# Performance work log

Measured on AMD Instinct MI355X. Metric: run time of the kernel, lower is better.

The kernel has to match this reference:

```python
import jax, jax.numpy as jnp
import numpy as np

B, L, H = 2, 2048, 1024
N_HEADS = 16
HEAD = H // N_HEADS
LN_EPS = 1e-12


def setup_inputs() -> dict:
    key = jax.random.key(0)
    ks = jax.random.split(key, 8)
    s = 1.0 / np.sqrt(H)
    return {
        "embeddings": jax.random.normal(ks[0], (B, L, H), dtype=jnp.float32),
        "mask": jnp.zeros((B, 1, 1, L), dtype=jnp.float32),
        "Wq": jax.random.normal(ks[1], (H, H), dtype=jnp.float32) * s,
        "bq": jnp.zeros((H,), dtype=jnp.float32),
        "Wk": jax.random.normal(ks[2], (H, H), dtype=jnp.float32) * s,
        "bk": jnp.zeros((H,), dtype=jnp.float32),
        "Wv": jax.random.normal(ks[3], (H, H), dtype=jnp.float32) * s,
        "bv": jnp.zeros((H,), dtype=jnp.float32),
        "Wo": jax.random.normal(ks[4], (H, H), dtype=jnp.float32) * s,
        "bo": jnp.zeros((H,), dtype=jnp.float32),
        "ln_gamma": jnp.ones((H,), dtype=jnp.float32),
        "ln_beta": jnp.zeros((H,), dtype=jnp.float32),
    }


def _layer_norm(x, gamma, beta):
    mu = jnp.mean(x, axis=-1, keepdims=True)
    var = jnp.mean(jnp.square(x - mu), axis=-1, keepdims=True)
    return (x - mu) * jax.lax.rsqrt(var + LN_EPS) * gamma + beta


def reference(embeddings, mask, Wq, bq, Wk, bk, Wv, bv, Wo, bo, ln_gamma, ln_beta):
    b, l, h = embeddings.shape
    # QKV projections, split heads -> [b, n_heads, l, head]
    def split_heads(x):
        return x.reshape(b, l, N_HEADS, HEAD).transpose(0, 2, 1, 3)
    q = split_heads(embeddings @ Wq + bq)
    k = split_heads(embeddings @ Wk + bk)
    v = split_heads(embeddings @ Wv + bv)
    # Faithful to source: energies use Q @ V^T, scaled by sqrt(n_heads)
    energies = jnp.einsum("bhqd,bhkd->bhqk", q, v) / np.sqrt(N_HEADS) + mask
    weights = jax.nn.softmax(energies, axis=3)
    # Faithful to source: attended = weights @ K
    attended = jnp.einsum("bhqk,bhkd->bhqd", weights, k)
    attended = attended.transpose(0, 2, 1, 3).reshape(b, l, h)
    # Residual feed-forward (BertSelfOutput style): dense + residual + LN
    out = attended @ Wo + bo
    return _layer_norm(out + embeddings, ln_gamma, ln_beta)
```

## Files before the change

kernel.cpp:

```cpp
#include <hip/hip_runtime.h>

#define LOG2E 1.44269504f
#define C_QSCALE 0.360673760f
#define C_SHIFT  34.6246810f
typedef unsigned short u16;
typedef short bf16x8 __attribute__((ext_vector_type(8)));
typedef float f32x4 __attribute__((ext_vector_type(4)));
typedef unsigned short u16x4 __attribute__((ext_vector_type(4)));

#define BB 2
#define LL 2048
#define HH 1024
#define NH 16
#define HD 64
#define ML (BB*LL)

__device__ __forceinline__ u16 f2bf(float f) {
  union { float f; unsigned u; } v; v.f = f;
  unsigned r = v.u + 0x7FFFu + ((v.u >> 16) & 1u);
  return (u16)(r >> 16);
}
__device__ __forceinline__ u16 f2bf_trunc(float f) {
  union { float f; unsigned u; } v; v.f = f;
  return (u16)(v.u >> 16);
}
__device__ __forceinline__ void gload_lds16(const u16* g, u16* l) {
  __builtin_amdgcn_global_load_lds((const __attribute__((address_space(1))) void*)g,
                                   (__attribute__((address_space(3))) void*)l, 16, 0, 0);
}

__global__ __launch_bounds__(256) void k_convert(const float* __restrict__ E, u16* __restrict__ X) {
  int idx = (blockIdx.x * 256 + threadIdx.x) * 8;
  float4 a = *(const float4*)(E + idx);
  float4 b = *(const float4*)(E + idx + 4);
  bf16x8 o;
  o[0]=f2bf(a.x); o[1]=f2bf(a.y); o[2]=f2bf(a.z); o[3]=f2bf(a.w);
  o[4]=f2bf(b.x); o[5]=f2bf(b.y); o[6]=f2bf(b.z); o[7]=f2bf(b.w);
  *(bf16x8*)(X + idx) = o;
}

__global__ __launch_bounds__(256) void k_transpose(const float* W0, const float* W1,
                                                   const float* W2, const float* W3,
                                                   u16* __restrict__ WT) {
  const float* W = (blockIdx.z==0)?W0:(blockIdx.z==1)?W1:(blockIdx.z==2)?W2:W3;
  u16* dst = WT + (size_t)blockIdx.z * HH * HH;
  __shared__ __align__(16) u16 T[64*72];
  int t = threadIdx.x;
  int n0 = blockIdx.x * 64, k0 = blockIdx.y * 64;
  int kl = t >> 2, nc = t & 3;
  #pragma unroll
  for (int u = 0; u < 4; ++u) {
    float4 v = *(const float4*)(W + (size_t)(k0 + kl) * HH + n0 + nc*16 + u*4);
    int nb = nc*16 + u*4;
    T[(nb+0)*72 + kl] = f2bf(v.x);
    T[(nb+1)*72 + kl] = f2bf(v.y);
    T[(nb+2)*72 + kl] = f2bf(v.z);
    T[(nb+3)*72 + kl] = f2bf(v.w);
  }
  __syncthreads();
  int nl = t >> 2, kc = (t & 3) * 16;
  #pragma unroll
  for (int e = 0; e < 2; ++e) {
    bf16x8 v = *(const bf16x8*)(T + nl*72 + kc + e*8);
    *(bf16x8*)(dst + (size_t)(n0+nl)*HH + k0 + kc + e*8) = v;
  }
}

__global__ __launch_bounds__(256) void k_gemm(const u16* __restrict__ A, const u16* __restrict__ Bt,
                                              const float* __restrict__ b0, const float* __restrict__ b1,
                                              const float* __restrict__ b2,
                                              u16* __restrict__ QH, u16* __restrict__ KV,
                                              float* __restrict__ outf, int mode) {
  __shared__ __align__(16) u16 As[128*32];
  __shared__ __align__(16) u16 Bs[128*32];
  int tid = threadIdx.x;
  int lane = tid & 63, w = tid >> 6;
  int c = lane & 15, g = lane >> 4;
  int bn0 = blockIdx.x * 128, bm0 = blockIdx.y * 128;
  int wm0 = (w >> 1) * 64, wn0 = (w & 1) * 64;
  f32x4 acc[4][4];
  #pragma unroll
  for (int mt = 0; mt < 4; ++mt)
    #pragma unroll
    for (int nt = 0; nt < 4; ++nt)
      acc[mt][nt] = (f32x4){0.f,0.f,0.f,0.f};

  for (int kt = 0; kt < 32; ++kt) {
    int k0 = kt * 32;
    __syncthreads();
    #pragma unroll
    for (int it = 0; it < 2; ++it) {
      int ch = tid + it*256;
      int row = ch >> 2, col = (ch & 3) * 8;
      gload_lds16(A  + (size_t)(bm0 + row) * HH + k0 + col, As + ch*8);
      gload_lds16(Bt + (size_t)(bn0 + row) * HH + k0 + col, Bs + ch*8);
    }
    __syncthreads();
    bf16x8 af[4], bfr[4];
    #pragma unroll
    for (int i = 0; i < 4; ++i) {
      af[i]  = *(const bf16x8*)(As + (wm0 + i*16 + c)*32 + g*8);
      bfr[i] = *(const bf16x8*)(Bs + (wn0 + i*16 + c)*32 + g*8);
    }
    #pragma unroll
    for (int mt = 0; mt < 4; ++mt)
      #pragma unroll
      for (int nt = 0; nt < 4; ++nt)
        acc[mt][nt] = __builtin_amdgcn_mfma_f32_16x16x32_bf16(af[mt], bfr[nt], acc[mt][nt], 0, 0, 0);
  }
  #pragma unroll
  for (int nt = 0; nt < 4; ++nt) {
    int n = bn0 + wn0 + nt*16 + c;
    if (mode == 1) {
      float bv = b0[n];
      #pragma unroll
      for (int mt = 0; mt < 4; ++mt) {
        int m0 = bm0 + wm0 + mt*16 + 4*g;
        #pragma unroll
        for (int r = 0; r < 4; ++r)
          outf[(size_t)(m0 + r) * HH + n] = acc[mt][nt][r] + bv;
      }
    } else {
      int z = n >> 10;
      int nn = n & 1023, h = nn >> 6, d = nn & 63;
      const float* bp = (z == 0) ? b0 : (z == 1) ? b1 : b2;
      float bv = bp[nn];
      #pragma unroll
      for (int mt = 0; mt < 4; ++mt) {
        int m0 = bm0 + wm0 + mt*16 + 4*g;
        int b = m0 >> 11;
        if (z == 0) {
          #pragma unroll
          for (int r = 0; r < 4; ++r) {
            int l = (m0 + r) & 2047;
            QH[(((size_t)(b*NH + h)) * LL + l) * HD + d] = f2bf(acc[mt][nt][r] + bv);
          }
        } else if (z == 1) {
          int keyl = m0 & 2047;
          int t = keyl >> 6, chunk = (keyl >> 3) & 7, s = keyl & 7;
          u16x4 pk;
          #pragma unroll
          for (int r = 0; r < 4; ++r) pk[r] = f2bf(acc[mt][nt][r] + bv);
          size_t addr = ((size_t)((b*NH + h)*32 + t))*8192 + d*64 + ((chunk ^ (d & 7))*8) + s;
          *(u16x4*)(KV + addr) = pk;
        } else {
          #pragma unroll
          for (int r = 0; r < 4; ++r) {
            int vl = (m0 + r) & 2047;
            int t = vl >> 6;
            size_t addr = ((size_t)((b*NH + h)*32 + t))*8192 + 4096
                        + (vl & 63)*64 + (((d >> 3) ^ (vl & 7))*8) + (d & 7);
            KV[addr] = f2bf(acc[mt][nt][r] + bv);
          }
        }
      }
    }
  }
}

__global__ __launch_bounds__(256) void k_attn(const u16* __restrict__ QH, const u16* __restrict__ KV,
                                              const float* __restrict__ mask, u16* __restrict__ ATT) {
  __shared__ __align__(16) u16 sKV[8192];
  __shared__ __align__(16) u16 sP[4][32*72];
  int tid = threadIdx.x;
  int lane = tid & 63, w = tid >> 6;
  int c = lane & 15, g = lane >> 4;
  int bh = blockIdx.y, b = bh >> 4, h = bh & 15;
  int q0 = blockIdx.x * 128 + w * 32;
  size_t qbase = (size_t)bh * LL * HD;
  const u16* kvg = KV + (size_t)bh * 32 * 8192;
  const float* mptr = mask + b * LL;

  bf16x8 aq[2][2];
  #pragma unroll
  for (int qi = 0; qi < 2; ++qi)
    #pragma unroll
    for (int ks = 0; ks < 2; ++ks)
      aq[qi][ks] = *(const bf16x8*)(QH + qbase + (size_t)(q0 + qi*16 + c) * HD + ks*32 + g*8);

  bf16x8 ones;
  #pragma unroll
  for (int i = 0; i < 8; ++i) ones[i] = (short)0x3F80;

  f32x4 O[2][4], lac[2];
  #pragma unroll
  for (int qi = 0; qi < 2; ++qi) {
    lac[qi] = (f32x4){0.f,0.f,0.f,0.f};
    #pragma unroll
    for (int dt = 0; dt < 4; ++dt) O[qi][dt] = (f32x4){0.f,0.f,0.f,0.f};
  }
  u16* pw = &sP[w][0];

  for (int t = 0; t < 32; ++t) {
    int kv0 = t * 64;
    __syncthreads();
    #pragma unroll
    for (int it = 0; it < 4; ++it) {
      int i = tid + it*256;
      gload_lds16(kvg + (size_t)t*8192 + i*8, sKV + i*8);
    }
    __syncthreads();

    #pragma unroll
    for (int nt = 0; nt < 4; ++nt) {
      int vrow = nt*16 + c;
      bf16x8 vb0 = *(const bf16x8*)(sKV + 4096 + vrow*64 + ((g ^ (c & 7))*8));
      bf16x8 vb1 = *(const bf16x8*)(sKV + 4096 + vrow*64 + (((4 + g) ^ (c & 7))*8));
      float mterm = fmaf(mptr[kv0 + nt*16 + c], LOG2E, -C_SHIFT);
      #pragma unroll
      for (int qi = 0; qi < 2; ++qi) {
        f32x4 sa = (f32x4){0.f,0.f,0.f,0.f};
        sa = __builtin_amdgcn_mfma_f32_16x16x32_bf16(aq[qi][0], vb0, sa, 0,0,0);
        sa = __builtin_amdgcn_mfma_f32_16x16x32_bf16(aq[qi][1], vb1, sa, 0,0,0);
        #pragma unroll
        for (int r = 0; r < 4; ++r) {
          float p = exp2f(fmaf(sa[r], C_QSCALE, mterm));
          pw[(qi*16 + 4*g + r)*72 + nt*16 + c] = f2bf_trunc(p);
        }
      }
    }
    bf16x8 ap[2][2];
    #pragma unroll
    for (int qi = 0; qi < 2; ++qi) {
      #pragma unroll
      for (int ks = 0; ks < 2; ++ks)
        ap[qi][ks] = *(const bf16x8*)(pw + (qi*16 + c)*72 + ks*32 + g*8);
      lac[qi] = __builtin_amdgcn_mfma_f32_16x16x32_bf16(ap[qi][0], ones, lac[qi], 0,0,0);
      lac[qi] = __builtin_amdgcn_mfma_f32_16x16x32_bf16(ap[qi][1], ones, lac[qi], 0,0,0);
    }
    #pragma unroll
    for (int dt = 0; dt < 4; ++dt) {
      int d = dt*16 + c;
      bf16x8 bk0 = *(const bf16x8*)(sKV + d*64 + ((g ^ (c & 7))*8));
      bf16x8 bk1 = *(const bf16x8*)(sKV + d*64 + (((4 + g) ^ (c & 7))*8));
      #pragma unroll
      for (int qi = 0; qi < 2; ++qi) {
        O[qi][dt] = __builtin_amdgcn_mfma_f32_16x16x32_bf16(ap[qi][0], bk0, O[qi][dt], 0,0,0);
        O[qi][dt] = __builtin_amdgcn_mfma_f32_16x16x32_bf16(ap[qi][1], bk1, O[qi][dt], 0,0,0);
      }
    }
  }
  #pragma unroll
  for (int qi = 0; qi < 2; ++qi)
    #pragma unroll
    for (int r = 0; r < 4; ++r) {
      float inv = 1.0f / lac[qi][r];
      int q = q0 + qi*16 + 4*g + r;
      #pragma unroll
      for (int dt = 0; dt < 4; ++dt)
        ATT[((size_t)(b*LL + q)) * HH + h*HD + dt*16 + c] = f2bf(O[qi][dt][r] * inv);
    }
}

__global__ __launch_bounds__(256) void k_ln(const float* __restrict__ OF, const float* __restrict__ E,
                                            const float* __restrict__ gamma, const float* __restrict__ beta,
                                            float* __restrict__ out) {
  int row = blockIdx.x;
  int tid = threadIdx.x, lane = tid & 63, w = tid >> 6;
  size_t basei = (size_t)row * HH + tid*4;
  float4 a = *(const float4*)(OF + basei);
  float4 e = *(const float4*)(E + basei);
  float x0 = a.x + e.x, x1 = a.y + e.y, x2 = a.z + e.z, x3 = a.w + e.w;
  float s1 = x0+x1+x2+x3;
  float s2 = x0*x0+x1*x1+x2*x2+x3*x3;
  #pragma unroll
  for (int off = 32; off; off >>= 1) { s1 += __shfl_xor(s1, off); s2 += __shfl_xor(s2, off); }
  __shared__ float r1[4], r2[4];
  if (lane == 0) { r1[w] = s1; r2[w] = s2; }
  __syncthreads();
  s1 = r1[0]+r1[1]+r1[2]+r1[3];
  s2 = r2[0]+r2[1]+r2[2]+r2[3];
  float mu = s1 * (1.0f/HH);
  float var = s2 * (1.0f/HH) - mu*mu;
  float rs = rsqrtf(fmaxf(var, 0.f) + 1e-12f);
  int colb = tid*4;
  float4 gm = *(const float4*)(gamma + colb);
  float4 bt = *(const float4*)(beta + colb);
  float4 o;
  o.x = (x0-mu)*rs*gm.x + bt.x;
  o.y = (x1-mu)*rs*gm.y + bt.y;
  o.z = (x2-mu)*rs*gm.z + bt.z;
  o.w = (x3-mu)*rs*gm.w + bt.w;
  *(float4*)(out + basei) = o;
}

extern "C" void kernel_launch(void* const* d_in, const int* in_sizes, int n_in,
                              void* d_out, int out_size, void* d_ws, size_t ws_size,
                              hipStream_t stream) {
  const float* E    = (const float*)d_in[0];
  const float* mask = (const float*)d_in[1];
  const float* Wq   = (const float*)d_in[2];
  const float* bq   = (const float*)d_in[3];
  const float* Wk   = (const float*)d_in[4];
  const float* bk   = (const float*)d_in[5];
  const float* Wv   = (const float*)d_in[6];
  const float* bv   = (const float*)d_in[7];
  const float* Wo   = (const float*)d_in[8];
  const float* bo   = (const float*)d_in[9];
  const float* gam  = (const float*)d_in[10];
  const float* bet  = (const float*)d_in[11];

  const size_t MH = (size_t)ML * HH;
  u16* XBF = (u16*)d_ws;
  u16* WT  = XBF + MH;
  u16* QH  = WT + 4*(size_t)HH*HH;
  u16* KV  = QH + MH;
  u16* ATT = KV + 2*MH;
  float* OF = (float*)QH;
  float* out = (float*)d_out;

  k_convert<<<dim3(ML*HH/(256*8)), 256, 0, stream>>>(E, XBF);
  k_transpose<<<dim3(16,16,4), 256, 0, stream>>>(Wq, Wk, Wv, Wo, WT);
  k_gemm<<<dim3(24,32), 256, 0, stream>>>(XBF, WT, bq, bk, bv, QH, KV, nullptr, 0);
  k_attn<<<dim3(16,32), 256, 0, stream>>>(QH, KV, mask, ATT);
  k_gemm<<<dim3(8,32), 256, 0, stream>>>(ATT, WT + 3*(size_t)HH*HH, bo, nullptr, nullptr,
                                         nullptr, nullptr, OF, 1);
  k_ln<<<dim3(ML), 256, 0, stream>>>(OF, E, gam, bet, out);
}
```

Measured before the change: 273.1 us.

## Double-buffer GEMM and attention loads, merge prep kernels, vectorize epilogue stores

Merges the bf16 conversion and weight transpose into one prep launch. Double-buffers the LDS tiles in the GEMM and the KV tiles in attention, so the next tile's global-to-LDS load overlaps the current tile's MFMA work and one barrier per iteration goes away. The GEMM swaps operands for the Q/V/output projections so the epilogue can write packed 4-wide stores. Attention is reworked to 16 queries per wave with twice the blocks, using transposed MFMA operands so outputs are stored as packed vectors. The costs are double the LDS footprint per block, and the prefetch is issued after only a single barrier, which may rely on implicit waits for the async loads to be safe.

```diff
diff --git a/kernel.cpp b/kernel.cpp
--- a/kernel.cpp
+++ b/kernel.cpp
@@ -29,24 +29,27 @@
                                    (__attribute__((address_space(3))) void*)l, 16, 0, 0);
 }
 
-__global__ __launch_bounds__(256) void k_convert(const float* __restrict__ E, u16* __restrict__ X) {
-  int idx = (blockIdx.x * 256 + threadIdx.x) * 8;
-  float4 a = *(const float4*)(E + idx);
-  float4 b = *(const float4*)(E + idx + 4);
-  bf16x8 o;
-  o[0]=f2bf(a.x); o[1]=f2bf(a.y); o[2]=f2bf(a.z); o[3]=f2bf(a.w);
-  o[4]=f2bf(b.x); o[5]=f2bf(b.y); o[6]=f2bf(b.z); o[7]=f2bf(b.w);
-  *(bf16x8*)(X + idx) = o;
-}
-
-__global__ __launch_bounds__(256) void k_transpose(const float* W0, const float* W1,
-                                                   const float* W2, const float* W3,
-                                                   u16* __restrict__ WT) {
-  const float* W = (blockIdx.z==0)?W0:(blockIdx.z==1)?W1:(blockIdx.z==2)?W2:W3;
-  u16* dst = WT + (size_t)blockIdx.z * HH * HH;
+__global__ __launch_bounds__(256) void k_prep(const float* __restrict__ E, u16* __restrict__ X,
+                                              const float* W0, const float* W1,
+                                              const float* W2, const float* W3,
+                                              u16* __restrict__ WT) {
   __shared__ __align__(16) u16 T[64*72];
+  if (blockIdx.x < 2048) {
+    int idx = (blockIdx.x * 256 + threadIdx.x) * 8;
+    float4 a = *(const float4*)(E + idx);
+    float4 b = *(const float4*)(E + idx + 4);
+    bf16x8 o;
+    o[0]=f2bf(a.x); o[1]=f2bf(a.y); o[2]=f2bf(a.z); o[3]=f2bf(a.w);
+    o[4]=f2bf(b.x); o[5]=f2bf(b.y); o[6]=f2bf(b.z); o[7]=f2bf(b.w);
+    *(bf16x8*)(X + idx) = o;
+    return;
+  }
+  int bz = blockIdx.x - 2048;
+  int z = bz >> 8, rem = bz & 255, bx = rem & 15, by = rem >> 4;
+  const float* W = (z==0)?W0:(z==1)?W1:(z==2)?W2:W3;
+  u16* dst = WT + (size_t)z * HH * HH;
   int t = threadIdx.x;
-  int n0 = blockIdx.x * 64, k0 = blockIdx.y * 64;
+  int n0 = bx * 64, k0 = by * 64;
   int kl = t >> 2, nc = t & 3;
   #pragma unroll
   for (int u = 0; u < 4; ++u) {
@@ -71,13 +74,20 @@
                                               const float* __restrict__ b2,
                                               u16* __restrict__ QH, u16* __restrict__ KV,
                                               float* __restrict__ outf, int mode) {
-  __shared__ __align__(16) u16 As[128*32];
-  __shared__ __align__(16) u16 Bs[128*32];
+  __shared__ __align__(16) u16 As[2][128*32];
+  __shared__ __align__(16) u16 Bs[2][128*32];
   int tid = threadIdx.x;
   int lane = tid & 63, w = tid >> 6;
   int c = lane & 15, g = lane >> 4;
   int bn0 = blockIdx.x * 128, bm0 = blockIdx.y * 128;
   int wm0 = (w >> 1) * 64, wn0 = (w & 1) * 64;
+  int z = bn0 >> 10;
+  bool swapd = (mode == 1) || (z != 1);
+  const u16* srcA = swapd ? Bt : A;
+  const u16* srcB = swapd ? A : Bt;
+  int baseA = swapd ? bn0 : bm0;
+  int baseB = swapd ? bm0 : bn0;
+
   f32x4 acc[4][4];
   #pragma unroll
   for (int mt = 0; mt < 4; ++mt)
@@ -85,22 +95,29 @@
     for (int nt = 0; nt < 4; ++nt)
       acc[mt][nt] = (f32x4){0.f,0.f,0.f,0.f};
 
+  #pragma unroll
+  for (int it = 0; it < 2; ++it) {
+    int ch = tid + it*256, row = ch >> 2, col = (ch & 3) * 8;
+    gload_lds16(srcA + (size_t)(baseA + row) * HH + col, &As[0][ch*8]);
+    gload_lds16(srcB + (size_t)(baseB + row) * HH + col, &Bs[0][ch*8]);
+  }
   for (int kt = 0; kt < 32; ++kt) {
-    int k0 = kt * 32;
     __syncthreads();
-    #pragma unroll
-    for (int it = 0; it < 2; ++it) {
-      int ch = tid + it*256;
-      int row = ch >> 2, col = (ch & 3) * 8;
-      gload_lds16(A  + (size_t)(bm0 + row) * HH + k0 + col, As + ch*8);
-      gload_lds16(Bt + (size_t)(bn0 + row) * HH + k0 + col, Bs + ch*8);
-    }
-    __syncthreads();
+    int cb = kt & 1;
+    if (kt < 31) {
+      int k0 = (kt + 1) * 32, nb = (kt + 1) & 1;
+      #pragma unroll
+      for (int it = 0; it < 2; ++it) {
+        int ch = tid + it*256, row = ch >> 2, col = (ch & 3) * 8;
+        gload_lds16(srcA + (size_t)(baseA + row) * HH + k0 + col, &As[nb][ch*8]);
+        gload_lds16(srcB + (size_t)(baseB + row) * HH + k0 + col, &Bs[nb][ch*8]);
+      }
+    }
     bf16x8 af[4], bfr[4];
     #pragma unroll
     for (int i = 0; i < 4; ++i) {
-      af[i]  = *(const bf16x8*)(As + (wm0 + i*16 + c)*32 + g*8);
-      bfr[i] = *(const bf16x8*)(Bs + (wn0 + i*16 + c)*32 + g*8);
+      af[i]  = *(const bf16x8*)(&As[cb][0] + (wm0 + i*16 + c)*32 + g*8);
+      bfr[i] = *(const bf16x8*)(&Bs[cb][0] + (wn0 + i*16 + c)*32 + g*8);
     }
     #pragma unroll
     for (int mt = 0; mt < 4; ++mt)
@@ -108,50 +125,62 @@
       for (int nt = 0; nt < 4; ++nt)
         acc[mt][nt] = __builtin_amdgcn_mfma_f32_16x16x32_bf16(af[mt], bfr[nt], acc[mt][nt], 0, 0, 0);
   }
-  #pragma unroll
-  for (int nt = 0; nt < 4; ++nt) {
-    int n = bn0 + wn0 + nt*16 + c;
-    if (mode == 1) {
-      float bv = b0[n];
+
+  if (mode == 1) {
+    #pragma unroll
+    for (int mt = 0; mt < 4; ++mt) {
+      int n0 = bn0 + wm0 + mt*16 + 4*g;
+      float4 bv = *(const float4*)(b0 + n0);
+      #pragma unroll
+      for (int nt = 0; nt < 4; ++nt) {
+        int tok = bm0 + wn0 + nt*16 + c;
+        float4 o;
+        o.x = acc[mt][nt][0] + bv.x;
+        o.y = acc[mt][nt][1] + bv.y;
+        o.z = acc[mt][nt][2] + bv.z;
+        o.w = acc[mt][nt][3] + bv.w;
+        *(float4*)(outf + (size_t)tok * HH + n0) = o;
+      }
+    }
+  } else if (z == 1) {
+    #pragma unroll
+    for (int nt = 0; nt < 4; ++nt) {
+      int n = bn0 + wn0 + nt*16 + c;
+      int nn = n & 1023, h = nn >> 6, d = nn & 63;
+      float bv = b1[nn];
       #pragma unroll
       for (int mt = 0; mt < 4; ++mt) {
         int m0 = bm0 + wm0 + mt*16 + 4*g;
+        int b = m0 >> 11, keyl = m0 & 2047;
+        int tt = keyl >> 6, chunk = (keyl >> 3) & 7, s = keyl & 7;
+        u16x4 pk;
         #pragma unroll
-        for (int r = 0; r < 4; ++r)
-          outf[(size_t)(m0 + r) * HH + n] = acc[mt][nt][r] + bv;
-      }
-    } else {
-      int z = n >> 10;
-      int nn = n & 1023, h = nn >> 6, d = nn & 63;
-      const float* bp = (z == 0) ? b0 : (z == 1) ? b1 : b2;
-      float bv = bp[nn];
-      #pragma unroll
-      for (int mt = 0; mt < 4; ++mt) {
-        int m0 = bm0 + wm0 + mt*16 + 4*g;
-        int b = m0 >> 11;
+        for (int r = 0; r < 4; ++r) pk[r] = f2bf(acc[mt][nt][r] + bv);
+        *(u16x4*)(KV + ((size_t)((b*NH + h)*32 + tt))*8192 + d*64 + ((chunk ^ (d & 7))*8) + s) = pk;
+      }
+    }
+  } else {
+    #pragma unroll
+    for (int mt = 0; mt < 4; ++mt) {
+      int nidx0 = bn0 + wm0 + mt*16 + 4*g;
+      int nn0 = nidx0 & 1023, h = nn0 >> 6, d0 = nn0 & 63;
+      const float* bp = (z == 0) ? b0 : b2;
+      float4 bv = *(const float4*)(bp + nn0);
+      #pragma unroll
+      for (int nt = 0; nt < 4; ++nt) {
+        int tok = bm0 + wn0 + nt*16 + c;
+        int b = tok >> 11, l = tok & 2047;
+        u16x4 o;
+        o[0] = f2bf(acc[mt][nt][0] + bv.x);
+        o[1] = f2bf(acc[mt][nt][1] + bv.y);
+        o[2] = f2bf(acc[mt][nt][2] + bv.z);
+        o[3] = f2bf(acc[mt][nt][3] + bv.w);
         if (z == 0) {
-          #pragma unroll
-          for (int r = 0; r < 4; ++r) {
-            int l = (m0 + r) & 2047;
-            QH[(((size_t)(b*NH + h)) * LL + l) * HD + d] = f2bf(acc[mt][nt][r] + bv);
-          }
-        } else if (z == 1) {
-          int keyl = m0 & 2047;
-          int t = keyl >> 6, chunk = (keyl >> 3) & 7, s = keyl & 7;
-          u16x4 pk;
-          #pragma unroll
-          for (int r = 0; r < 4; ++r) pk[r] = f2bf(acc[mt][nt][r] + bv);
-          size_t addr = ((size_t)((b*NH + h)*32 + t))*8192 + d*64 + ((chunk ^ (d & 7))*8) + s;
-          *(u16x4*)(KV + addr) = pk;
+          *(u16x4*)(QH + (((size_t)(b*NH + h)) * LL + l) * HD + d0) = o;
         } else {
-          #pragma unroll
-          for (int r = 0; r < 4; ++r) {
-            int vl = (m0 + r) & 2047;
-            int t = vl >> 6;
-            size_t addr = ((size_t)((b*NH + h)*32 + t))*8192 + 4096
-                        + (vl & 63)*64 + (((d >> 3) ^ (vl & 7))*8) + (d & 7);
-            KV[addr] = f2bf(acc[mt][nt][r] + bv);
-          }
+          int tt = l >> 6;
+          *(u16x4*)(KV + ((size_t)((b*NH + h)*32 + tt))*8192 + 4096
+                    + (l & 63)*64 + (((d0 >> 3) ^ (l & 7))*8) + (d0 & 7)) = o;
         }
       }
     }
@@ -160,96 +189,84 @@
 
 __global__ __launch_bounds__(256) void k_attn(const u16* __restrict__ QH, const u16* __restrict__ KV,
                                               const float* __restrict__ mask, u16* __restrict__ ATT) {
-  __shared__ __align__(16) u16 sKV[8192];
-  __shared__ __align__(16) u16 sP[4][32*72];
+  __shared__ __align__(16) u16 sKV[2][8192];
+  __shared__ __align__(16) u16 sP[4][16*72];
   int tid = threadIdx.x;
   int lane = tid & 63, w = tid >> 6;
   int c = lane & 15, g = lane >> 4;
   int bh = blockIdx.y, b = bh >> 4, h = bh & 15;
-  int q0 = blockIdx.x * 128 + w * 32;
+  int q0 = blockIdx.x * 64 + w * 16;
   size_t qbase = (size_t)bh * LL * HD;
   const u16* kvg = KV + (size_t)bh * 32 * 8192;
   const float* mptr = mask + b * LL;
 
-  bf16x8 aq[2][2];
-  #pragma unroll
-  for (int qi = 0; qi < 2; ++qi)
-    #pragma unroll
-    for (int ks = 0; ks < 2; ++ks)
-      aq[qi][ks] = *(const bf16x8*)(QH + qbase + (size_t)(q0 + qi*16 + c) * HD + ks*32 + g*8);
+  bf16x8 aq[2];
+  aq[0] = *(const bf16x8*)(QH + qbase + (size_t)(q0 + c) * HD + g*8);
+  aq[1] = *(const bf16x8*)(QH + qbase + (size_t)(q0 + c) * HD + 32 + g*8);
 
   bf16x8 ones;
   #pragma unroll
   for (int i = 0; i < 8; ++i) ones[i] = (short)0x3F80;
 
-  f32x4 O[2][4], lac[2];
-  #pragma unroll
-  for (int qi = 0; qi < 2; ++qi) {
-    lac[qi] = (f32x4){0.f,0.f,0.f,0.f};
-    #pragma unroll
-    for (int dt = 0; dt < 4; ++dt) O[qi][dt] = (f32x4){0.f,0.f,0.f,0.f};
-  }
+  f32x4 O[4], lac;
+  lac = (f32x4){0.f,0.f,0.f,0.f};
+  #pragma unroll
+  for (int dt = 0; dt < 4; ++dt) O[dt] = (f32x4){0.f,0.f,0.f,0.f};
   u16* pw = &sP[w][0];
 
+  #pragma unroll
+  for (int it = 0; it < 4; ++it) {
+    int i = (tid + it*256) * 8;
+    gload_lds16(kvg + i, &sKV[0][0] + i);
+  }
   for (int t = 0; t < 32; ++t) {
+    __syncthreads();
+    const u16* cur = &sKV[t & 1][0];
+    if (t < 31) {
+      const u16* src = kvg + (size_t)(t + 1) * 8192;
+      u16* dst = &sKV[(t + 1) & 1][0];
+      #pragma unroll
+      for (int it = 0; it < 4; ++it) {
+        int i = (tid + it*256) * 8;
+        gload_lds16(src + i, dst + i);
+      }
+    }
     int kv0 = t * 64;
-    __syncthreads();
-    #pragma unroll
-    for (int it = 0; it < 4; ++it) {
-      int i = tid + it*256;
-      gload_lds16(kvg + (size_t)t*8192 + i*8, sKV + i*8);
-    }
-    __syncthreads();
-
     #pragma unroll
     for (int nt = 0; nt < 4; ++nt) {
       int vrow = nt*16 + c;
-      bf16x8 vb0 = *(const bf16x8*)(sKV + 4096 + vrow*64 + ((g ^ (c & 7))*8));
-      bf16x8 vb1 = *(const bf16x8*)(sKV + 4096 + vrow*64 + (((4 + g) ^ (c & 7))*8));
-      float mterm = fmaf(mptr[kv0 + nt*16 + c], LOG2E, -C_SHIFT);
-      #pragma unroll
-      for (int qi = 0; qi < 2; ++qi) {
-        f32x4 sa = (f32x4){0.f,0.f,0.f,0.f};
-        sa = __builtin_amdgcn_mfma_f32_16x16x32_bf16(aq[qi][0], vb0, sa, 0,0,0);
-        sa = __builtin_amdgcn_mfma_f32_16x16x32_bf16(aq[qi][1], vb1, sa, 0,0,0);
-        #pragma unroll
-        for (int r = 0; r < 4; ++r) {
-          float p = exp2f(fmaf(sa[r], C_QSCALE, mterm));
-          pw[(qi*16 + 4*g + r)*72 + nt*16 + c] = f2bf_trunc(p);
-        }
-      }
-    }
-    bf16x8 ap[2][2];
-    #pragma unroll
-    for (int qi = 0; qi < 2; ++qi) {
-      #pragma unroll
-      for (int ks = 0; ks < 2; ++ks)
-        ap[qi][ks] = *(const bf16x8*)(pw + (qi*16 + c)*72 + ks*32 + g*8);
-      lac[qi] = __builtin_amdgcn_mfma_f32_16x16x32_bf16(ap[qi][0], ones, lac[qi], 0,0,0);
-      lac[qi] = __builtin_amdgcn_mfma_f32_16x16x32_bf16(ap[qi][1], ones, lac[qi], 0,0,0);
-    }
+      bf16x8 vb0 = *(const bf16x8*)(cur + 4096 + vrow*64 + ((g ^ (c & 7))*8));
+      bf16x8 vb1 = *(const bf16x8*)(cur + 4096 + vrow*64 + (((4 + g) ^ (c & 7))*8));
+      float mterm = fmaf(mptr[kv0 + vrow], LOG2E, -C_SHIFT);
+      f32x4 sa = (f32x4){0.f,0.f,0.f,0.f};
+      sa = __builtin_amdgcn_mfma_f32_16x16x32_bf16(aq[0], vb0, sa, 0,0,0);
+      sa = __builtin_amdgcn_mfma_f32_16x16x32_bf16(aq[1], vb1, sa, 0,0,0);
+      #pragma unroll
+      for (int r = 0; r < 4; ++r)
+        pw[(4*g + r)*72 + nt*16 + c] = f2bf_trunc(exp2f(fmaf(sa[r], C_QSCALE, mterm)));
+    }
+    bf16x8 ap0 = *(const bf16x8*)(pw + c*72 + g*8);
+    bf16x8 ap1 = *(const bf16x8*)(pw + c*72 + 32 + g*8);
+    lac = __builtin_amdgcn_mfma_f32_16x16x32_bf16(ones, ap0, lac, 0,0,0);
+    lac = __builtin_amdgcn_mfma_f32_16x16x32_bf16(ones, ap1, lac, 0,0,0);
     #pragma unroll
     for (int dt = 0; dt < 4; ++dt) {
       int d = dt*16 + c;
-      bf16x8 bk0 = *(const bf16x8*)(sKV + d*64 + ((g ^ (c & 7))*8));
-      bf16x8 bk1 = *(const bf16x8*)(sKV + d*64 + (((4 + g) ^ (c & 7))*8));
-      #pragma unroll
-      for (int qi = 0; qi < 2; ++qi) {
-        O[qi][dt] = __builtin_amdgcn_mfma_f32_16x16x32_bf16(ap[qi][0], bk0, O[qi][dt], 0,0,0);
-        O[qi][dt] = __builtin_amdgcn_mfma_f32_16x16x32_bf16(ap[qi][1], bk1, O[qi][dt], 0,0,0);
-      }
-    }
-  }
-  #pragma unroll
-  for (int qi = 0; qi < 2; ++qi)
-    #pragma unroll
-    for (int r = 0; r < 4; ++r) {
-      float inv = 1.0f / lac[qi][r];
-      int q = q0 + qi*16 + 4*g + r;
-      #pragma unroll
-      for (int dt = 0; dt < 4; ++dt)
-        ATT[((size_t)(b*LL + q)) * HH + h*HD + dt*16 + c] = f2bf(O[qi][dt][r] * inv);
-    }
+      bf16x8 bk0 = *(const bf16x8*)(cur + d*64 + ((g ^ (c & 7))*8));
+      bf16x8 bk1 = *(const bf16x8*)(cur + d*64 + (((4 + g) ^ (c & 7))*8));
+      O[dt] = __builtin_amdgcn_mfma_f32_16x16x32_bf16(bk0, ap0, O[dt], 0,0,0);
+      O[dt] = __builtin_amdgcn_mfma_f32_16x16x32_bf16(bk1, ap1, O[dt], 0,0,0);
+    }
+  }
+  float inv = 1.0f / lac[0];
+  size_t orow = ((size_t)(b*LL + q0 + c)) * HH + h*HD;
+  #pragma unroll
+  for (int dt = 0; dt < 4; ++dt) {
+    u16x4 o;
+    #pragma unroll
+    for (int r = 0; r < 4; ++r) o[r] = f2bf(O[dt][r] * inv);
+    *(u16x4*)(ATT + orow + dt*16 + 4*g) = o;
+  }
 }
 
 __global__ __launch_bounds__(256) void k_ln(const float* __restrict__ OF, const float* __restrict__ E,
@@ -309,10 +326,9 @@
   float* OF = (float*)QH;
   float* out = (float*)d_out;
 
-  k_convert<<<dim3(ML*HH/(256*8)), 256, 0, stream>>>(E, XBF);
-  k_transpose<<<dim3(16,16,4), 256, 0, stream>>>(Wq, Wk, Wv, Wo, WT);
+  k_prep<<<dim3(3072), 256, 0, stream>>>(E, XBF, Wq, Wk, Wv, Wo, WT);
   k_gemm<<<dim3(24,32), 256, 0, stream>>>(XBF, WT, bq, bk, bv, QH, KV, nullptr, 0);
-  k_attn<<<dim3(16,32), 256, 0, stream>>>(QH, KV, mask, ATT);
+  k_attn<<<dim3(32,32), 256, 0, stream>>>(QH, KV, mask, ATT);
   k_gemm<<<dim3(8,32), 256, 0, stream>>>(ATT, WT + 3*(size_t)HH*HH, bo, nullptr, nullptr,
                                          nullptr, nullptr, OF, 1);
   k_ln<<<dim3(ML), 256, 0, stream>>>(OF, E, gam, bet, out);
```

Result: no change. 271.8 us (-0.5%).
